# Performance work log

Measured on AMD Instinct MI355X. Metric: run time of the kernel, lower is better.

The kernel has to match this reference:

```python
import jax, jax.numpy as jnp
import numpy as np

N_NODES = 100000
N_EDGES = 1600000
IN_CH = 256
HID = 128   # latent_dim * 2
LAT = 64    # latent_dim


def _gcn_conv(x, W, b, src, dst, n_nodes):
    """PyG GCNConv: linear -> symmetric degree-norm scatter-add -> bias.
    src/dst already include self-loops."""
    h = x @ W.T                                             # [N, out]
    deg = jax.ops.segment_sum(jnp.ones_like(dst, dtype=h.dtype), dst,
                              num_segments=n_nodes)          # in-degree incl. self-loop
    dinv = jnp.where(deg > 0, jax.lax.rsqrt(deg), 0.0)
    norm = dinv[src] * dinv[dst]                             # [E]
    msg = h[src] * norm[:, None]                             # gather + scale, [E, out]
    out = jax.ops.segment_sum(msg, dst, num_segments=n_nodes)  # scatter-add
    return out + b


def setup_inputs() -> dict:
    key = jax.random.key(0)
    k1, k2, k3, k4, k5, k6 = jax.random.split(key, 6)
    x = jax.random.normal(k1, (N_NODES, IN_CH), dtype=jnp.float32)
    edge_index = jax.random.randint(k2, (2, N_EDGES), 0, N_NODES, dtype=jnp.int64)
    # Glorot-ish init for linear weights, zero bias (PyG default)
    W1 = jax.random.normal(k3, (HID, IN_CH), dtype=jnp.float32) / np.sqrt(IN_CH)
    b1 = jnp.zeros((HID,), dtype=jnp.float32)
    W2 = jax.random.normal(k4, (LAT, HID), dtype=jnp.float32) / np.sqrt(HID)
    b2 = jnp.zeros((LAT,), dtype=jnp.float32)
    return {"x": x, "edge_index": edge_index, "W1": W1, "b1": b1, "W2": W2, "b2": b2}


def reference(x, edge_index, W1, b1, W2, b2):
    n = x.shape[0]
    # add self-loops (PyG GCNConv default add_self_loops=True)
    loop = jnp.arange(n, dtype=edge_index.dtype)
    src = jnp.concatenate([edge_index[0], loop])
    dst = jnp.concatenate([edge_index[1], loop])
    h = jax.nn.relu(_gcn_conv(x, W1, b1, src, dst, n))
    return _gcn_conv(h, W2, b2, src, dst, n)
```

## Files before the change

kernel.cpp:

```cpp
#include <hip/hip_runtime.h>
#include <math.h>

constexpr int IN_CH = 256;
constexpr int HID   = 128;
constexpr int LAT   = 64;

constexpr int SBN    = 1024;
constexpr int SB_CAP = 18432;
constexpr int EPB    = 8192;
constexpr int HCAP   = 9472;

typedef unsigned short u16;
typedef unsigned int   u32;
typedef unsigned char  u8;
typedef __bf16  bf16x8 __attribute__((ext_vector_type(8)));
typedef float   f32x4  __attribute__((ext_vector_type(4)));

__device__ inline u16 f2bf(float f) {
    unsigned u = __float_as_uint(f);
    unsigned r = u + 0x7FFF + ((u >> 16) & 1);
    return (u16)(r >> 16);
}
__device__ inline float bf2f(u16 h) {
    return __uint_as_float((unsigned)h << 16);
}


__global__ void k_zero(int* p, int n) {
    int i = blockIdx.x * blockDim.x + threadIdx.x;
    if (i < n) p[i] = 0;
}

__launch_bounds__(512)
__global__ void k_bin_sb(const int* __restrict__ esrc, const int* __restrict__ edst,
                         int* __restrict__ sb_fill, u32* __restrict__ sbe,
                         int E, int NSB) {
    __shared__ u32 sorted[EPB];
    __shared__ u8  ssb[EPB];
    __shared__ int cnt[128], sc[128], excl[128], fil[128], off[128];

    const int t  = threadIdx.x;
    const int e0 = blockIdx.x * EPB;

    for (int j = t; j < 128; j += 512) { cnt[j] = 0; fil[j] = 0; }
    __syncthreads();

#pragma unroll
    for (int it = 0; it < EPB / 512; ++it) {
        int e = e0 + it * 512 + t;
        if (e < E) atomicAdd(&cnt[edst[e] >> 10], 1);
    }
    __syncthreads();

    if (t < 128) sc[t] = cnt[t];
    __syncthreads();
#pragma unroll
    for (int o = 1; o < 128; o <<= 1) {
        int u = 0;
        if (t < 128 && t >= o) u = sc[t - o];
        __syncthreads();
        if (t < 128) sc[t] += u;
        __syncthreads();
    }
    if (t < 128) excl[t] = sc[t] - cnt[t];
    if (t < NSB) off[t] = atomicAdd(&sb_fill[t], cnt[t]);
    __syncthreads();

#pragma unroll
    for (int it = 0; it < EPB / 512; ++it) {
        int e = e0 + it * 512 + t;
        if (e < E) {
            int d  = edst[e];
            int sb = d >> 10;
            int pos = excl[sb] + atomicAdd(&fil[sb], 1);
            sorted[pos] = (u32)esrc[e] | ((u32)(d & 1023) << 17);
            ssb[pos]    = (u8)sb;
        }
    }
    __syncthreads();

    int mtot = sc[127];
    for (int i = t; i < mtot; i += 512) {
        int sb = ssb[i];
        int o  = off[sb] + (i - excl[sb]);
        if (o < SB_CAP) sbe[(size_t)sb * SB_CAP + o] = sorted[i];
    }
}

__launch_bounds__(512)
__global__ void k_sbsort(const int* __restrict__ sb_fill, const u32* __restrict__ sbe,
                         int* __restrict__ csr, int* __restrict__ row_ptr,
                         int* __restrict__ row_end, float* __restrict__ dinv, int N) {
    __shared__ int cnt[SBN];
    __shared__ int exclh[512];
    __shared__ int fillb[512];
    __shared__ int lsrc[HCAP];
    __shared__ int wsum[8];
    __shared__ int sh_h1base, sh_mtot;

    const int t    = threadIdx.x;
    const int sb   = blockIdx.x >> 1;
    const int half = blockIdx.x & 1;
    const int m    = min(sb_fill[sb], SB_CAP);
    const size_t base = (size_t)sb * SB_CAP;
    const int node0 = sb * SBN;

    for (int j = t; j < SBN; j += 512) cnt[j] = 0;
    fillb[t & 511] = 0;
    __syncthreads();

    for (int i = t; i < m; i += 512)
        atomicAdd(&cnt[sbe[base + i] >> 17], 1);
    __syncthreads();

    int c0 = cnt[2 * t], c1 = cnt[2 * t + 1];
    int p  = c0 + c1;
    int lane = t & 63, wid = t >> 6;
    int v = p;
#pragma unroll
    for (int o = 1; o < 64; o <<= 1) {
        int u = __shfl_up(v, o, 64);
        if (lane >= o) v += u;
    }
    if (lane == 63) wsum[wid] = v;
    __syncthreads();
    int woff = 0;
#pragma unroll
    for (int w = 0; w < 8; ++w) if (w < wid) woff += wsum[w];
    int incl = woff + v;
    int eP   = incl - p;
    if (t == 511) sh_mtot = incl;
    if (t == 256) sh_h1base = eP;

#pragma unroll
    for (int q = 0; q < 2; ++q) {
        int j  = 2 * t + q;
        int ex = q ? (eP + c0) : eP;
        int cc = q ? c1 : c0;
        if ((j >> 9) == half) {
            exclh[j & 511] = ex;
            int node = node0 + j;
            if (node < N) {
                row_ptr[node] = (int)base + ex;
                row_end[node] = (int)base + ex + cc;
                dinv[node]    = rsqrtf((float)(cc + 1));
            }
        }
    }
    __syncthreads();

    const int hb = (half == 0) ? 0 : sh_h1base;
    int mh = (half == 0) ? sh_h1base : (sh_mtot - sh_h1base);

    for (int i = t; i < m; i += 512) {
        u32 p2  = sbe[base + i];
        int d10 = p2 >> 17;
        if ((d10 >> 9) == half) {
            int slot = atomicAdd(&fillb[d10 & 511], 1);
            int pos  = exclh[d10 & 511] - hb + slot;
            if (pos < HCAP) lsrc[pos] = (int)(p2 & 0x1FFFF);
        }
    }
    __syncthreads();

    if (mh > HCAP) mh = HCAP;
    for (int i = t; i < mh; i += 512) csr[base + hb + i] = lsrc[i];
}


__global__ void k_split_w(const float* __restrict__ W, u16* __restrict__ Wh,
                          u16* __restrict__ Wl, int n) {
    int i = blockIdx.x * blockDim.x + threadIdx.x;
    if (i < n) {
        float v = W[i];
        u16 h = f2bf(v);
        Wh[i] = h;
        Wl[i] = f2bf(v - bf2f(h));
    }
}


template<int K, int NOUT, int BM, int WAVES_N, bool A_BF16, typename AT>
__device__ inline void gemm_body(int bid,
                                 const AT* __restrict__ A,
                                 const u16* __restrict__ Wh,
                                 const u16* __restrict__ Wl,
                                 const float* __restrict__ dinv,
                                 u16* __restrict__ h_out,
                                 int M) {
    constexpr int BK = 32, LDT = 40, THREADS = 512;
    constexpr int WAVES_M  = 8 / WAVES_N;
    constexpr int WM       = BM / WAVES_M;
    constexpr int WN       = NOUT / WAVES_N;
    constexpr int MF       = WM / 16;
    constexpr int NF       = WN / 16;

    __shared__ u16 Ah[BM][LDT];
    __shared__ u16 Al[A_BF16 ? 1 : BM][A_BF16 ? 1 : LDT];
    __shared__ u16 Bh[NOUT][LDT], Bl[NOUT][LDT];

    const int t    = threadIdx.x;
    const int lane = t & 63;
    const int wid  = t >> 6;
    const int wm   = (wid / WAVES_N) * WM;
    const int wn   = (wid % WAVES_N) * WN;
    const int lr   = lane & 15;
    const int lk   = (lane >> 4) * 8;
    const int row0 = bid * BM;

    f32x4 acc[MF][NF];
#pragma unroll
    for (int i = 0; i < MF; ++i)
#pragma unroll
        for (int j = 0; j < NF; ++j) acc[i][j] = (f32x4)(0.f);

    for (int k0 = 0; k0 < K; k0 += BK) {
#pragma unroll
        for (int q = t; q < BM * BK / 4; q += THREADS) {
            int r  = q >> 3;
            int c4 = (q & 7) * 4;
            int gr = row0 + r;
            if constexpr (A_BF16) {
                ushort4 hv = make_ushort4(0, 0, 0, 0);
                if (gr < M) hv = *(const ushort4*)&((const u16*)A)[(size_t)gr * K + k0 + c4];
                *(ushort4*)&Ah[r][c4] = hv;
            } else {
                float4 v = make_float4(0.f, 0.f, 0.f, 0.f);
                if (gr < M) v = *(const float4*)&((const float*)A)[(size_t)gr * K + k0 + c4];
                ushort4 hi, lo;
                hi.x = f2bf(v.x); lo.x = f2bf(v.x - bf2f(hi.x));
                hi.y = f2bf(v.y); lo.y = f2bf(v.y - bf2f(hi.y));
                hi.z = f2bf(v.z); lo.z = f2bf(v.z - bf2f(hi.z));
                hi.w = f2bf(v.w); lo.w = f2bf(v.w - bf2f(hi.w));
                *(ushort4*)&Ah[r][c4] = hi;
                *(ushort4*)&Al[r][c4] = lo;
            }
        }
#pragma unroll
        for (int q = t; q < NOUT * BK / 4; q += THREADS) {
            int r  = q >> 3;
            int c4 = (q & 7) * 4;
            *(ushort4*)&Bh[r][c4] = *(const ushort4*)&Wh[(size_t)r * K + k0 + c4];
            *(ushort4*)&Bl[r][c4] = *(const ushort4*)&Wl[(size_t)r * K + k0 + c4];
        }
        __syncthreads();

        bf16x8 ah[MF], al[MF], bh[NF], bl[NF];
#pragma unroll
        for (int mf = 0; mf < MF; ++mf) {
            ah[mf] = *(const bf16x8*)&Ah[wm + mf * 16 + lr][lk];
            if constexpr (!A_BF16)
                al[mf] = *(const bf16x8*)&Al[wm + mf * 16 + lr][lk];
        }
#pragma unroll
        for (int nf = 0; nf < NF; ++nf) {
            bh[nf] = *(const bf16x8*)&Bh[wn + nf * 16 + lr][lk];
            bl[nf] = *(const bf16x8*)&Bl[wn + nf * 16 + lr][lk];
        }
#pragma unroll
        for (int mf = 0; mf < MF; ++mf)
#pragma unroll
            for (int nf = 0; nf < NF; ++nf) {
                acc[mf][nf] = __builtin_amdgcn_mfma_f32_16x16x32_bf16(ah[mf], bh[nf], acc[mf][nf], 0, 0, 0);
                acc[mf][nf] = __builtin_amdgcn_mfma_f32_16x16x32_bf16(ah[mf], bl[nf], acc[mf][nf], 0, 0, 0);
                if constexpr (!A_BF16)
                    acc[mf][nf] = __builtin_amdgcn_mfma_f32_16x16x32_bf16(al[mf], bh[nf], acc[mf][nf], 0, 0, 0);
            }
        __syncthreads();
    }

#pragma unroll
    for (int mf = 0; mf < MF; ++mf) {
#pragma unroll
        for (int r = 0; r < 4; ++r) {
            int grow = row0 + wm + mf * 16 + (lane >> 4) * 4 + r;
            if (grow < M) {
                float dv = dinv[grow];
#pragma unroll
                for (int nf = 0; nf < NF; ++nf)
                    h_out[(size_t)grow * NOUT + wn + nf * 16 + lr] = f2bf(acc[mf][nf][r] * dv);
            }
        }
    }
}

__launch_bounds__(512, 8)
__global__ void k_gemm1(const float* __restrict__ A,
                        const u16* __restrict__ Wh, const u16* __restrict__ Wl,
                        const float* __restrict__ dinv, u16* __restrict__ h_out, int M) {
    gemm_body<IN_CH, HID, 32, 8, false>(blockIdx.x, A, Wh, Wl, dinv, h_out, M);
}

__launch_bounds__(512, 4)
__global__ void k_gemm2(const u16* __restrict__ A,
                        const u16* __restrict__ Wh, const u16* __restrict__ Wl,
                        const float* __restrict__ dinv, u16* __restrict__ h_out, int M) {
    gemm_body<HID, LAT, 64, 2, true>(blockIdx.x, A, Wh, Wl, dinv, h_out, M);
}


__device__ inline void acc8(float* a, uint4 v) {
    a[0] += __uint_as_float(v.x << 16);
    a[1] += __uint_as_float(v.x & 0xFFFF0000u);
    a[2] += __uint_as_float(v.y << 16);
    a[3] += __uint_as_float(v.y & 0xFFFF0000u);
    a[4] += __uint_as_float(v.z << 16);
    a[5] += __uint_as_float(v.z & 0xFFFF0000u);
    a[6] += __uint_as_float(v.w << 16);
    a[7] += __uint_as_float(v.w & 0xFFFF0000u);
}

template<int C, bool RELU, bool OUT_BF16>
__global__ void k_aggregate(const int* __restrict__ row_ptr,
                            const int* __restrict__ row_end,
                            const int* __restrict__ csr,
                            const u16* __restrict__ h,
                            const float* __restrict__ dinv,
                            const float* __restrict__ bias,
                            void* __restrict__ out_v, int n) {
    constexpr int QSHIFT = (C == 128) ? 4 : 3;
    long long tid = (long long)blockIdx.x * blockDim.x + threadIdx.x;
    int node = (int)(tid >> QSHIFT);
    if (node >= n) return;
    int c = ((int)tid & ((1 << QSHIFT) - 1)) * 8;

    int k   = row_ptr[node];
    int end = row_end[node];

    float a[8] = {0.f, 0.f, 0.f, 0.f, 0.f, 0.f, 0.f, 0.f};
    acc8(a, *(const uint4*)&h[(size_t)node * C + c]);

    for (; k + 8 <= end; k += 8) {
        int s0 = csr[k],     s1 = csr[k + 1], s2 = csr[k + 2], s3 = csr[k + 3];
        int s4 = csr[k + 4], s5 = csr[k + 5], s6 = csr[k + 6], s7 = csr[k + 7];
        uint4 v0 = *(const uint4*)&h[(size_t)s0 * C + c];
        uint4 v1 = *(const uint4*)&h[(size_t)s1 * C + c];
        uint4 v2 = *(const uint4*)&h[(size_t)s2 * C + c];
        uint4 v3 = *(const uint4*)&h[(size_t)s3 * C + c];
        uint4 v4 = *(const uint4*)&h[(size_t)s4 * C + c];
        uint4 v5 = *(const uint4*)&h[(size_t)s5 * C + c];
        uint4 v6 = *(const uint4*)&h[(size_t)s6 * C + c];
        uint4 v7 = *(const uint4*)&h[(size_t)s7 * C + c];
        acc8(a, v0); acc8(a, v1); acc8(a, v2); acc8(a, v3);
        acc8(a, v4); acc8(a, v5); acc8(a, v6); acc8(a, v7);
    }
    if (k + 4 <= end) {
        int s0 = csr[k], s1 = csr[k + 1], s2 = csr[k + 2], s3 = csr[k + 3];
        uint4 v0 = *(const uint4*)&h[(size_t)s0 * C + c];
        uint4 v1 = *(const uint4*)&h[(size_t)s1 * C + c];
        uint4 v2 = *(const uint4*)&h[(size_t)s2 * C + c];
        uint4 v3 = *(const uint4*)&h[(size_t)s3 * C + c];
        acc8(a, v0); acc8(a, v1); acc8(a, v2); acc8(a, v3);
        k += 4;
    }
    for (; k < end; ++k) {
        int s0 = csr[k];
        acc8(a, *(const uint4*)&h[(size_t)s0 * C + c]);
    }

    float dvn = dinv[node];
    float4 b0 = *(const float4*)&bias[c];
    float4 b1 = *(const float4*)&bias[c + 4];
    float o[8];
    o[0] = fmaf(a[0], dvn, b0.x);
    o[1] = fmaf(a[1], dvn, b0.y);
    o[2] = fmaf(a[2], dvn, b0.z);
    o[3] = fmaf(a[3], dvn, b0.w);
    o[4] = fmaf(a[4], dvn, b1.x);
    o[5] = fmaf(a[5], dvn, b1.y);
    o[6] = fmaf(a[6], dvn, b1.z);
    o[7] = fmaf(a[7], dvn, b1.w);
    if (RELU) {
#pragma unroll
        for (int j = 0; j < 8; ++j) o[j] = fmaxf(o[j], 0.f);
    }
    if (OUT_BF16) {
        u16 r[8];
#pragma unroll
        for (int j = 0; j < 8; ++j) r[j] = f2bf(o[j]);
        *(uint4*)&((u16*)out_v)[(size_t)node * C + c] = *(const uint4*)r;
    } else {
        float* out = (float*)out_v;
        *(f32x4*)&out[(size_t)node * C + c]     = *(const f32x4*)&o[0];
        *(f32x4*)&out[(size_t)node * C + c + 4] = *(const f32x4*)&o[4];
    }
}


extern "C" void kernel_launch(void* const* d_in, const int* in_sizes, int n_in,
                              void* d_out, int out_size, void* d_ws, size_t ws_size,
                              hipStream_t stream) {
    const float* x   = (const float*)d_in[0];
    const int*   ei  = (const int*)d_in[1];
    const float* W1  = (const float*)d_in[2];
    const float* b1  = (const float*)d_in[3];
    const float* W2  = (const float*)d_in[4];
    const float* b2  = (const float*)d_in[5];
    float*       out = (float*)d_out;

    const int N = in_sizes[0] / IN_CH;
    const int E = in_sizes[1] / 2;
    const int* esrc = ei;
    const int* edst = ei + E;

    const int NSB = (N + SBN - 1) / SBN;
    const int NBB = (E + EPB - 1) / EPB;
    const int GB1 = (N + 31) / 32;
    const int GB2 = (N + 63) / 64;

    char* ws = (char*)d_ws;
    int*   sb_fill = (int*)ws;    ws += (size_t)((NSB + 31) & ~31) * 4;
    u32*   sbe     = (u32*)ws;    ws += (size_t)NSB * SB_CAP * 4;
    int*   csr     = (int*)ws;    ws += (size_t)NSB * SB_CAP * 4;
    int*   row_ptr = (int*)ws;    ws += (size_t)N * 4;
    int*   row_end = (int*)ws;    ws += (size_t)N * 4;
    float* dinv    = (float*)ws;  ws += (size_t)N * 4;
    u16*   W1h     = (u16*)ws;    ws += (size_t)HID * IN_CH * 2;
    u16*   W1l     = (u16*)ws;    ws += (size_t)HID * IN_CH * 2;
    u16*   W2h     = (u16*)ws;    ws += (size_t)LAT * HID * 2;
    u16*   W2l     = (u16*)ws;    ws += (size_t)LAT * HID * 2;
    u16*   h1      = (u16*)ws;    ws += (size_t)N * HID * 2;
    u16*   h2      = (u16*)ws;    ws += (size_t)N * LAT * 2;
    u16*   out1    = (u16*)ws;    ws += (size_t)N * HID * 2;

    dim3 blk(256);

    k_zero   <<<1, 128, 0, stream>>>(sb_fill, NSB);
    k_split_w<<<(HID * IN_CH + 255) / 256, blk, 0, stream>>>(W1, W1h, W1l, HID * IN_CH);
    k_split_w<<<(LAT * HID + 255) / 256, blk, 0, stream>>>(W2, W2h, W2l, LAT * HID);

    k_bin_sb<<<NBB, dim3(512), 0, stream>>>(esrc, edst, sb_fill, sbe, E, NSB);
    k_sbsort<<<NSB * 2, dim3(512), 0, stream>>>(sb_fill, sbe, csr, row_ptr, row_end, dinv, N);

    k_gemm1<<<GB1, dim3(512), 0, stream>>>(x, W1h, W1l, dinv, h1, N);
    {
        long long tot = (long long)N * 16;
        k_aggregate<HID, true, true><<<(unsigned)((tot + 255) / 256), blk, 0, stream>>>(
            row_ptr, row_end, csr, h1, dinv, b1, out1, N);
    }

    k_gemm2<<<GB2, dim3(512), 0, stream>>>(out1, W2h, W2l, dinv, h2, N);
    {
        long long tot = (long long)N * 8;
        k_aggregate<LAT, false, false><<<(unsigned)((tot + 255) / 256), blk, 0, stream>>>(
            row_ptr, row_end, csr, h2, dinv, b2, out, N);
    }
}
```

Baseline: 215.6 us.

## Pre-split x into bf16 hi/lo and stream GEMM tiles via global_load_lds

Converts x into bf16 hi/lo arrays inside the edge-binning kernel, so the fp32 split runs alongside binning instead of inside the GEMM. Both GEMMs now load A and W tiles with direct global-to-LDS loads (16 bytes per lane) using unpadded LDS tiles, BM is fixed at 64, and GEMM2 gets higher occupancy bounds. This removes register staging and conversion work from the GEMM inner loop, but adds a 100MB extra write and read of Xh/Xl. Unpadded LDS rows may cause bank conflicts, and A rows past M are no longer bounds-guarded (N=100000 is not a multiple of 64), so the last tile reads past the end of the array.

```diff
diff --git a/kernel.cpp b/kernel.cpp
--- a/kernel.cpp
+++ b/kernel.cpp
@@ -25,6 +25,13 @@
     return __uint_as_float((unsigned)h << 16);
 }
 
+__device__ inline void gload_lds16(const u16* g, u16* lds) {
+    __builtin_amdgcn_global_load_lds(
+        (const __attribute__((address_space(1))) void*)g,
+        (__attribute__((address_space(3))) void*)lds,
+        16, 0, 0);
+}
+
 
 __global__ void k_zero(int* p, int n) {
     int i = blockIdx.x * blockDim.x + threadIdx.x;
@@ -34,7 +41,9 @@
 __launch_bounds__(512)
 __global__ void k_bin_sb(const int* __restrict__ esrc, const int* __restrict__ edst,
                          int* __restrict__ sb_fill, u32* __restrict__ sbe,
-                         int E, int NSB) {
+                         const float* __restrict__ x, u16* __restrict__ Xh,
+                         u16* __restrict__ Xl,
+                         int E, int NSB, int N) {
     __shared__ u32 sorted[EPB];
     __shared__ u8  ssb[EPB];
     __shared__ int cnt[128], sc[128], excl[128], fil[128], off[128];
@@ -84,6 +93,24 @@
         int sb = ssb[i];
         int o  = off[sb] + (i - excl[sb]);
         if (o < SB_CAP) sbe[(size_t)sb * SB_CAP + o] = sorted[i];
+    }
+
+    const int total = N * (IN_CH / 8);
+    const int stride = (int)gridDim.x * 512;
+    for (int q = (int)blockIdx.x * 512 + t; q < total; q += stride) {
+        int r  = q >> 5;
+        int c8 = (q & 31) * 8;
+        float f[8];
+        *(float4*)&f[0] = *(const float4*)&x[(size_t)r * IN_CH + c8];
+        *(float4*)&f[4] = *(const float4*)&x[(size_t)r * IN_CH + c8 + 4];
+        u16 hh[8], ll[8];
+#pragma unroll
+        for (int j = 0; j < 8; ++j) {
+            hh[j] = f2bf(f[j]);
+            ll[j] = f2bf(f[j] - bf2f(hh[j]));
+        }
+        *(uint4*)&Xh[(size_t)r * IN_CH + c8] = *(const uint4*)hh;
+        *(uint4*)&Xl[(size_t)r * IN_CH + c8] = *(const uint4*)ll;
     }
 }
 
@@ -180,24 +207,30 @@
 }
 
 
-template<int K, int NOUT, int BM, int WAVES_N, bool A_BF16, typename AT>
+template<int K, int NOUT, bool HAS_AL>
 __device__ inline void gemm_body(int bid,
-                                 const AT* __restrict__ A,
-                                 const u16* __restrict__ Wh,
-                                 const u16* __restrict__ Wl,
+                                 const u16* __restrict__ Ahg,
+                                 const u16* __restrict__ Alg,
+                                 const u16* __restrict__ Whg,
+                                 const u16* __restrict__ Wlg,
                                  const float* __restrict__ dinv,
                                  u16* __restrict__ h_out,
                                  int M) {
-    constexpr int BK = 32, LDT = 40, THREADS = 512;
-    constexpr int WAVES_M  = 8 / WAVES_N;
-    constexpr int WM       = BM / WAVES_M;
-    constexpr int WN       = NOUT / WAVES_N;
-    constexpr int MF       = WM / 16;
-    constexpr int NF       = WN / 16;
-
-    __shared__ u16 Ah[BM][LDT];
-    __shared__ u16 Al[A_BF16 ? 1 : BM][A_BF16 ? 1 : LDT];
-    __shared__ u16 Bh[NOUT][LDT], Bl[NOUT][LDT];
+    constexpr int BM = 64, BK = 32;
+    constexpr int WAVES_N = (NOUT == 128) ? 4 : 2;
+    constexpr int WAVES_M = 8 / WAVES_N;
+    constexpr int WM      = BM / WAVES_M;
+    constexpr int WN      = NOUT / WAVES_N;
+    constexpr int MF      = WM / 16;
+    constexpr int NF      = WN / 16;
+    constexpr int AT      = BM / 16;
+    constexpr int BT      = NOUT / 16;
+    constexpr int NA      = AT * (HAS_AL ? 2 : 1);
+    constexpr int NT      = NA + 2 * BT;
+
+    __shared__ u16 Ah[BM][BK];
+    __shared__ u16 Al[HAS_AL ? BM : 1][BK];
+    __shared__ u16 Bh[NOUT][BK], Bl[NOUT][BK];
 
     const int t    = threadIdx.x;
     const int lane = t & 63;
@@ -208,6 +241,9 @@
     const int lk   = (lane >> 4) * 8;
     const int row0 = bid * BM;
 
+    const int lrow = lane >> 2;
+    const int lch  = (lane & 3) * 8;
+
     f32x4 acc[MF][NF];
 #pragma unroll
     for (int i = 0; i < MF; ++i)
@@ -216,32 +252,25 @@
 
     for (int k0 = 0; k0 < K; k0 += BK) {
 #pragma unroll
-        for (int q = t; q < BM * BK / 4; q += THREADS) {
-            int r  = q >> 3;
-            int c4 = (q & 7) * 4;
-            int gr = row0 + r;
-            if constexpr (A_BF16) {
-                ushort4 hv = make_ushort4(0, 0, 0, 0);
-                if (gr < M) hv = *(const ushort4*)&((const u16*)A)[(size_t)gr * K + k0 + c4];
-                *(ushort4*)&Ah[r][c4] = hv;
+        for (int tau = wid; tau < NT; tau += 8) {
+            const u16* g;
+            u16* l;
+            if (tau < AT) {
+                g = Ahg + (size_t)(row0 + tau * 16 + lrow) * K + k0 + lch;
+                l = &Ah[tau * 16][0];
+            } else if (HAS_AL && tau < 2 * AT) {
+                g = Alg + (size_t)(row0 + (tau - AT) * 16 + lrow) * K + k0 + lch;
+                l = &Al[(tau - AT) * 16][0];
+            } else if (tau < NA + BT) {
+                int tb = tau - NA;
+                g = Whg + (size_t)(tb * 16 + lrow) * K + k0 + lch;
+                l = &Bh[tb * 16][0];
             } else {
-                float4 v = make_float4(0.f, 0.f, 0.f, 0.f);
-                if (gr < M) v = *(const float4*)&((const float*)A)[(size_t)gr * K + k0 + c4];
-                ushort4 hi, lo;
-                hi.x = f2bf(v.x); lo.x = f2bf(v.x - bf2f(hi.x));
-                hi.y = f2bf(v.y); lo.y = f2bf(v.y - bf2f(hi.y));
-                hi.z = f2bf(v.z); lo.z = f2bf(v.z - bf2f(hi.z));
-                hi.w = f2bf(v.w); lo.w = f2bf(v.w - bf2f(hi.w));
-                *(ushort4*)&Ah[r][c4] = hi;
-                *(ushort4*)&Al[r][c4] = lo;
+                int tb = tau - NA - BT;
+                g = Wlg + (size_t)(tb * 16 + lrow) * K + k0 + lch;
+                l = &Bl[tb * 16][0];
             }
-        }
-#pragma unroll
-        for (int q = t; q < NOUT * BK / 4; q += THREADS) {
-            int r  = q >> 3;
-            int c4 = (q & 7) * 4;
-            *(ushort4*)&Bh[r][c4] = *(const ushort4*)&Wh[(size_t)r * K + k0 + c4];
-            *(ushort4*)&Bl[r][c4] = *(const ushort4*)&Wl[(size_t)r * K + k0 + c4];
+            gload_lds16(g, l);
         }
         __syncthreads();
 
@@ -249,7 +278,7 @@
 #pragma unroll
         for (int mf = 0; mf < MF; ++mf) {
             ah[mf] = *(const bf16x8*)&Ah[wm + mf * 16 + lr][lk];
-            if constexpr (!A_BF16)
+            if constexpr (HAS_AL)
                 al[mf] = *(const bf16x8*)&Al[wm + mf * 16 + lr][lk];
         }
 #pragma unroll
@@ -263,7 +292,7 @@
             for (int nf = 0; nf < NF; ++nf) {
                 acc[mf][nf] = __builtin_amdgcn_mfma_f32_16x16x32_bf16(ah[mf], bh[nf], acc[mf][nf], 0, 0, 0);
                 acc[mf][nf] = __builtin_amdgcn_mfma_f32_16x16x32_bf16(ah[mf], bl[nf], acc[mf][nf], 0, 0, 0);
-                if constexpr (!A_BF16)
+                if constexpr (HAS_AL)
                     acc[mf][nf] = __builtin_amdgcn_mfma_f32_16x16x32_bf16(al[mf], bh[nf], acc[mf][nf], 0, 0, 0);
             }
         __syncthreads();
@@ -285,17 +314,17 @@
 }
 
 __launch_bounds__(512, 8)
-__global__ void k_gemm1(const float* __restrict__ A,
+__global__ void k_gemm1(const u16* __restrict__ Xh, const u16* __restrict__ Xl,
                         const u16* __restrict__ Wh, const u16* __restrict__ Wl,
                         const float* __restrict__ dinv, u16* __restrict__ h_out, int M) {
-    gemm_body<IN_CH, HID, 32, 8, false>(blockIdx.x, A, Wh, Wl, dinv, h_out, M);
-}
-
-__launch_bounds__(512, 4)
+    gemm_body<IN_CH, HID, true>(blockIdx.x, Xh, Xl, Wh, Wl, dinv, h_out, M);
+}
+
+__launch_bounds__(512, 8)
 __global__ void k_gemm2(const u16* __restrict__ A,
                         const u16* __restrict__ Wh, const u16* __restrict__ Wl,
                         const float* __restrict__ dinv, u16* __restrict__ h_out, int M) {
-    gemm_body<HID, LAT, 64, 2, true>(blockIdx.x, A, Wh, Wl, dinv, h_out, M);
+    gemm_body<HID, LAT, false>(blockIdx.x, A, nullptr, Wh, Wl, dinv, h_out, M);
 }
 
 
@@ -405,8 +434,7 @@
 
     const int NSB = (N + SBN - 1) / SBN;
     const int NBB = (E + EPB - 1) / EPB;
-    const int GB1 = (N + 31) / 32;
-    const int GB2 = (N + 63) / 64;
+    const int GB  = (N + 63) / 64;
 
     char* ws = (char*)d_ws;
     int*   sb_fill = (int*)ws;    ws += (size_t)((NSB + 31) & ~31) * 4;
@@ -415,13 +443,15 @@
     int*   row_ptr = (int*)ws;    ws += (size_t)N * 4;
     int*   row_end = (int*)ws;    ws += (size_t)N * 4;
     float* dinv    = (float*)ws;  ws += (size_t)N * 4;
+    u16*   Xh      = (u16*)ws;    ws += (size_t)N * IN_CH * 2;
+    u16*   Xl      = (u16*)ws;    ws += (size_t)N * IN_CH * 2;
     u16*   W1h     = (u16*)ws;    ws += (size_t)HID * IN_CH * 2;
     u16*   W1l     = (u16*)ws;    ws += (size_t)HID * IN_CH * 2;
     u16*   W2h     = (u16*)ws;    ws += (size_t)LAT * HID * 2;
     u16*   W2l     = (u16*)ws;    ws += (size_t)LAT * HID * 2;
     u16*   h1      = (u16*)ws;    ws += (size_t)N * HID * 2;
+    u16*   out1    = (u16*)ws;    ws += (size_t)N * HID * 2;
     u16*   h2      = (u16*)ws;    ws += (size_t)N * LAT * 2;
-    u16*   out1    = (u16*)ws;    ws += (size_t)N * HID * 2;
 
     dim3 blk(256);
 
@@ -429,17 +459,17 @@
     k_split_w<<<(HID * IN_CH + 255) / 256, blk, 0, stream>>>(W1, W1h, W1l, HID * IN_CH);
     k_split_w<<<(LAT * HID + 255) / 256, blk, 0, stream>>>(W2, W2h, W2l, LAT * HID);
 
-    k_bin_sb<<<NBB, dim3(512), 0, stream>>>(esrc, edst, sb_fill, sbe, E, NSB);
+    k_bin_sb<<<NBB, dim3(512), 0, stream>>>(esrc, edst, sb_fill, sbe, x, Xh, Xl, E, NSB, N);
     k_sbsort<<<NSB * 2, dim3(512), 0, stream>>>(sb_fill, sbe, csr, row_ptr, row_end, dinv, N);
 
-    k_gemm1<<<GB1, dim3(512), 0, stream>>>(x, W1h, W1l, dinv, h1, N);
+    k_gemm1<<<GB, dim3(512), 0, stream>>>(Xh, Xl, W1h, W1l, dinv, h1, N);
     {
         long long tot = (long long)N * 16;
         k_aggregate<HID, true, true><<<(unsigned)((tot + 255) / 256), blk, 0, stream>>>(
             row_ptr, row_end, csr, h1, dinv, b1, out1, N);
     }
 
-    k_gemm2<<<GB2, dim3(512), 0, stream>>>(out1, W2h, W2l, dinv, h2, N);
+    k_gemm2<<<GB, dim3(512), 0, stream>>>(out1, W2h, W2l, dinv, h2, N);
     {
         long long tot = (long long)N * 8;
         k_aggregate<LAT, false, false><<<(unsigned)((tot + 255) / 256), blk, 0, stream>>>(
```

Result: slower. 237.6 us (+10.2%).
